# Optimization experiments

Measured on AMD Instinct MI355X. Metric: run time of the kernel, lower is better.

Reference implementation:

```python
import jax, jax.numpy as jnp
import numpy as np

N, E = 10000, 320000
C_IN, C_OUT = 256, 128
EPS = 1e-5


def _p(key, shape, scale=0.02):
    return (jax.random.normal(key, shape, dtype=jnp.float32) * scale)


def setup_inputs() -> dict:
    key = jax.random.key(0)
    ks = jax.random.split(key, 16)
    inp = {
        "x": jax.random.normal(ks[0], (N, C_IN), dtype=jnp.float32),
        "edge_index": jax.random.randint(ks[1], (2, E), 0, N, dtype=jnp.int64),
        # GCNConv weights (stored [in, out] so forward is x @ W)
        "W1": _p(ks[2], (C_IN, C_OUT)), "b1": jnp.zeros((C_OUT,), jnp.float32),
        "W2": _p(ks[3], (C_OUT, C_OUT)), "b2": jnp.zeros((C_OUT,), jnp.float32),
        # LayerNorms
        "ln1_g": jnp.ones((C_OUT,), jnp.float32), "ln1_b": jnp.zeros((C_OUT,), jnp.float32),
        "ln2_g": jnp.ones((C_OUT,), jnp.float32), "ln2_b": jnp.zeros((C_OUT,), jnp.float32),
        # Attention QKV
        "Wq": _p(ks[4], (C_OUT, C_OUT)), "bq": jnp.zeros((C_OUT,), jnp.float32),
        "Wk": _p(ks[5], (C_OUT, C_OUT)), "bk": jnp.zeros((C_OUT,), jnp.float32),
        "Wv": _p(ks[6], (C_OUT, C_OUT)), "bv": jnp.zeros((C_OUT,), jnp.float32),
        # shortcut Linear (in_channels != out_channels)
        "Ws": _p(ks[7], (C_IN, C_OUT)), "bs": jnp.zeros((C_OUT,), jnp.float32),
    }
    return inp


def _gcn_conv(x, W, b, src, dst, n_nodes):
    # PyG GCNConv: h = x W; add self loops; sym-normalized scatter aggregation.
    h = x @ W  # [N, out]
    loop = jnp.arange(n_nodes, dtype=src.dtype)
    s = jnp.concatenate([src, loop])
    d = jnp.concatenate([dst, loop])
    deg = jax.ops.segment_sum(jnp.ones_like(d, dtype=h.dtype), d, num_segments=n_nodes)
    dis = jnp.where(deg > 0, jax.lax.rsqrt(deg), 0.0)  # deg^-1/2
    norm = dis[s] * dis[d]  # [E+N]
    agg = jax.ops.segment_sum(h[s] * norm[:, None], d, num_segments=n_nodes)
    return agg + b


def _layer_norm(x, g, b):
    mu = jnp.mean(x, axis=-1, keepdims=True)
    var = jnp.var(x, axis=-1, keepdims=True)
    return (x - mu) * jax.lax.rsqrt(var + EPS) * g + b


def reference(x, edge_index, W1, b1, W2, b2, ln1_g, ln1_b, ln2_g, ln2_b,
              Wq, bq, Wk, bk, Wv, bv, Ws, bs):
    src, dst = edge_index[0], edge_index[1]
    n = x.shape[0]
    identity = x @ Ws + bs
    out = _gcn_conv(x, W1, b1, src, dst, n)
    out = jax.nn.silu(_layer_norm(out, ln1_g, ln1_b))  # dropout = identity (eval)
    out = _gcn_conv(out, W2, b2, src, dst, n)
    out = _layer_norm(out, ln2_g, ln2_b)
    # dense self-attention over all nodes
    q = out @ Wq + bq
    k = out @ Wk + bk
    v = out @ Wv + bv
    scale = np.sqrt(out.shape[-1]).astype(np.float32)
    attn = jax.nn.softmax(q @ k.T / scale, axis=-1)  # [N, N]
    out = attn @ v + out
    return jax.nn.silu(out + identity)
```

## Files before the change

kernel.cpp:

```cpp
#include <hip/hip_runtime.h>
#include <hip/hip_bf16.h>

typedef unsigned short u16;
typedef unsigned int u32;
typedef __bf16 bf16x8 __attribute__((ext_vector_type(8)));
typedef float f32x4 __attribute__((ext_vector_type(4)));

#define MFMA16(a, b, c) __builtin_amdgcn_mfma_f32_16x16x32_bf16(a, b, c, 0, 0, 0)

static __device__ __forceinline__ u16 f2b(float f) {
  u32 u = __float_as_uint(f);
  return (u16)((u + 0x7FFFu + ((u >> 16) & 1u)) >> 16);
}
static __device__ __forceinline__ float blo(u32 u) { return __uint_as_float(u << 16); }
static __device__ __forceinline__ float bhi(u32 u) { return __uint_as_float(u & 0xffff0000u); }

static __device__ __forceinline__ void async_copy16(void* lds, const void* gp) {
  __builtin_amdgcn_global_load_lds(
      (const __attribute__((address_space(1))) unsigned int*)gp,
      (__attribute__((address_space(3))) unsigned int*)lds, 16, 0, 0);
}

__global__ void degi_kernel(const int* __restrict__ dst, int* __restrict__ degi, int E) {
  int e = blockIdx.x * 256 + threadIdx.x;
  if (e < E) atomicAdd(&degi[dst[e]], 1);
}

__global__ void dis_start_kernel(const int* __restrict__ degi, float* __restrict__ d,
                                 int* __restrict__ startb, int* __restrict__ counter, int N) {
  int i = blockIdx.x * 256 + threadIdx.x;
  if (i < N) {
    int dg = degi[i];
    d[i] = rsqrtf((float)dg + 1.0f);
    startb[i] = atomicAdd(counter, dg);
  }
}

__global__ void fill_kernel(const int* __restrict__ src, const int* __restrict__ dst,
                            const int* __restrict__ startb, int* __restrict__ cursor,
                            int* __restrict__ adj, int E) {
  int e = blockIdx.x * 256 + threadIdx.x;
  if (e < E) {
    int d = dst[e];
    int p = atomicAdd(&cursor[d], 1);
    adj[startb[d] + p] = src[e];
  }
}

__global__ void cast_all_kernel(const float* __restrict__ x, u16* __restrict__ xb, int n4,
                                const float* __restrict__ W1, const float* __restrict__ Ws,
                                const float* __restrict__ W2, const float* __restrict__ Wq,
                                const float* __restrict__ Wk, const float* __restrict__ Wv,
                                u16* __restrict__ out) {
  int t = blockIdx.x * 256 + threadIdx.x;
  if (t < n4) {
    float4 v = *(const float4*)&x[t * 4];
    ushort4 o;
    o.x = f2b(v.x); o.y = f2b(v.y); o.z = f2b(v.z); o.w = f2b(v.w);
    *(ushort4*)&xb[t * 4] = o;
    return;
  }
  int u = t - n4;
  if (u >= 131072) return;
  const float* src; int K, base, loc;
  if (u < 65536) {
    if (u < 32768) { src = W1; base = 0; } else { src = Ws; base = 32768; }
    loc = u - base; K = 256;
  } else {
    int seg = (u - 65536) >> 14;
    src = (seg == 0) ? W2 : (seg == 1) ? Wq : (seg == 2) ? Wk : Wv;
    base = 65536 + seg * 16384; loc = u & 16383; K = 128;
  }
  int k = loc >> 7, c = loc & 127;
  out[base + c * K + k] = f2b(src[loc]);
}

__global__ __launch_bounds__(64) void bgemm_dual(
    const u16* __restrict__ A, const u16* __restrict__ Wa, const u16* __restrict__ Wb,
    const float* __restrict__ bsb, u16* __restrict__ outa, float* __restrict__ outb, int M)
{
  int lane = threadIdx.x;
  int col = lane & 15, quad = lane >> 4;
  int row0 = blockIdx.x * 16;
  int cb = blockIdx.y * 64;
  int ar = row0 + col; if (ar > M - 1) ar = M - 1;
  const u16* ap = A + (size_t)ar * 256 + quad * 8;
  f32x4 Oa[4], Ob[4];
#pragma unroll
  for (int i = 0; i < 4; i++) {
    Oa[i][0] = 0.f; Oa[i][1] = 0.f; Oa[i][2] = 0.f; Oa[i][3] = 0.f;
    Ob[i] = Oa[i];
  }
#pragma unroll
  for (int k0 = 0; k0 < 256; k0 += 32) {
    bf16x8 aA = *(const bf16x8*)(ap + k0);
#pragma unroll
    for (int nb = 0; nb < 4; nb++) {
      size_t wofs = (size_t)(cb + nb * 16 + col) * 256 + k0 + quad * 8;
      Oa[nb] = MFMA16(aA, *(const bf16x8*)(Wa + wofs), Oa[nb]);
      Ob[nb] = MFMA16(aA, *(const bf16x8*)(Wb + wofs), Ob[nb]);
    }
  }
#pragma unroll
  for (int nb = 0; nb < 4; nb++) {
    int ch = cb + nb * 16 + col;
    float bv = bsb[ch];
#pragma unroll
    for (int r = 0; r < 4; r++) {
      int row = row0 + quad * 4 + r;
      if (row >= M) continue;
      outa[(size_t)row * 128 + ch] = f2b(Oa[nb][r]);
      outb[(size_t)row * 128 + ch] = Ob[nb][r] + bv;
    }
  }
}

__global__ __launch_bounds__(64) void bgemm_single(
    const u16* __restrict__ A, const u16* __restrict__ Wt, u16* __restrict__ outa, int M)
{
  int lane = threadIdx.x;
  int col = lane & 15, quad = lane >> 4;
  int row0 = blockIdx.x * 16;
  int cb = blockIdx.y * 64;
  int ar = row0 + col; if (ar > M - 1) ar = M - 1;
  const u16* ap = A + (size_t)ar * 128 + quad * 8;
  f32x4 O[4];
#pragma unroll
  for (int i = 0; i < 4; i++) { O[i][0] = 0.f; O[i][1] = 0.f; O[i][2] = 0.f; O[i][3] = 0.f; }
#pragma unroll
  for (int k0 = 0; k0 < 128; k0 += 32) {
    bf16x8 aA = *(const bf16x8*)(ap + k0);
#pragma unroll
    for (int nb = 0; nb < 4; nb++) {
      O[nb] = MFMA16(aA, *(const bf16x8*)(Wt + (size_t)(cb + nb * 16 + col) * 128 + k0 + quad * 8), O[nb]);
    }
  }
#pragma unroll
  for (int nb = 0; nb < 4; nb++) {
    int ch = cb + nb * 16 + col;
#pragma unroll
    for (int r = 0; r < 4; r++) {
      int row = row0 + quad * 4 + r;
      if (row >= M) continue;
      outa[(size_t)row * 128 + ch] = f2b(O[nb][r]);
    }
  }
}

__global__ __launch_bounds__(64) void bgemm_qkv(
    const u16* __restrict__ A, const u16* __restrict__ Wqt, const u16* __restrict__ Wkt,
    const u16* __restrict__ Wvt, const float* __restrict__ bq, const float* __restrict__ bk,
    const float* __restrict__ bv, u16* __restrict__ q_out, u16* __restrict__ k_out,
    u16* __restrict__ v_out, int M, int NP, float qscale)
{
  int lane = threadIdx.x;
  int col = lane & 15, quad = lane >> 4;
  int row0 = blockIdx.x * 16;
  int cb = blockIdx.y * 64;
  int ar = row0 + col; if (ar > M - 1) ar = M - 1;
  const u16* ap = A + (size_t)ar * 128 + quad * 8;
  f32x4 Oq[4], Ok[4], Ov[4];
#pragma unroll
  for (int i = 0; i < 4; i++) {
    Oq[i][0] = 0.f; Oq[i][1] = 0.f; Oq[i][2] = 0.f; Oq[i][3] = 0.f;
    Ok[i] = Oq[i]; Ov[i] = Oq[i];
  }
#pragma unroll
  for (int k0 = 0; k0 < 128; k0 += 32) {
    bf16x8 aA = *(const bf16x8*)(ap + k0);
#pragma unroll
    for (int nb = 0; nb < 4; nb++) {
      size_t wofs = (size_t)(cb + nb * 16 + col) * 128 + k0 + quad * 8;
      Oq[nb] = MFMA16(aA, *(const bf16x8*)(Wqt + wofs), Oq[nb]);
      Ok[nb] = MFMA16(aA, *(const bf16x8*)(Wkt + wofs), Ok[nb]);
      Ov[nb] = MFMA16(aA, *(const bf16x8*)(Wvt + wofs), Ov[nb]);
    }
  }
#pragma unroll
  for (int nb = 0; nb < 4; nb++) {
    int ch = cb + nb * 16 + col;
    float bqv = bq[ch], bkv = bk[ch], bvv = bv[ch];
#pragma unroll
    for (int r = 0; r < 4; r++) {
      int row = row0 + quad * 4 + r;
      if (row >= M) continue;
      q_out[(size_t)row * 128 + ch] = f2b((Oq[nb][r] + bqv) * qscale);
      k_out[(size_t)row * 128 + ch] = f2b(Ok[nb][r] + bkv);
      v_out[(size_t)ch * NP + row] = f2b(Ov[nb][r] + bvv);
    }
  }
}

__global__ __launch_bounds__(256) void gather_ln(
    const u16* __restrict__ h, const float* __restrict__ dis,
    const int* __restrict__ adj, const int* __restrict__ startb, const int* __restrict__ degi,
    const float* __restrict__ bias, const float* __restrict__ g, const float* __restrict__ beta,
    float* __restrict__ out, u16* __restrict__ outb, int N, int do_silu)
{
  int row = blockIdx.x * 4 + (threadIdx.x >> 6);
  int lane = threadIdx.x & 63;
  if (row >= N) return;
  int st = startb[row], dg = degi[row];
  int c2 = lane * 2;
  float v0 = 0.f, v1 = 0.f;
  for (int base = 0; base < dg; base += 64) {
    int nb = min(64, dg - base);
    int myadj = 0; float mydis = 0.f;
    if (lane < nb) { myadj = adj[st + base + lane]; mydis = dis[myadj]; }
    int jj = 0;
    for (; jj + 4 <= nb; jj += 4) {
      int s0 = __shfl(myadj, jj), s1 = __shfl(myadj, jj + 1);
      int s2 = __shfl(myadj, jj + 2), s3 = __shfl(myadj, jj + 3);
      float w0 = __shfl(mydis, jj), w1 = __shfl(mydis, jj + 1);
      float w2 = __shfl(mydis, jj + 2), w3 = __shfl(mydis, jj + 3);
      u32 a0 = *(const u32*)&h[(size_t)s0 * 128 + c2];
      u32 a1 = *(const u32*)&h[(size_t)s1 * 128 + c2];
      u32 a2 = *(const u32*)&h[(size_t)s2 * 128 + c2];
      u32 a3 = *(const u32*)&h[(size_t)s3 * 128 + c2];
      v0 += w0 * blo(a0); v1 += w0 * bhi(a0);
      v0 += w1 * blo(a1); v1 += w1 * bhi(a1);
      v0 += w2 * blo(a2); v1 += w2 * bhi(a2);
      v0 += w3 * blo(a3); v1 += w3 * bhi(a3);
    }
    for (; jj < nb; jj++) {
      int s = __shfl(myadj, jj);
      float wv = __shfl(mydis, jj);
      u32 a = *(const u32*)&h[(size_t)s * 128 + c2];
      v0 += wv * blo(a); v1 += wv * bhi(a);
    }
  }
  float dd = dis[row];
  u32 aself = *(const u32*)&h[(size_t)row * 128 + c2];
  v0 = (v0 + dd * blo(aself)) * dd + bias[c2];
  v1 = (v1 + dd * bhi(aself)) * dd + bias[c2 + 1];
  float s = v0 + v1;
#pragma unroll
  for (int d = 32; d > 0; d >>= 1) s += __shfl_xor(s, d, 64);
  float mu = s * (1.0f / 128.0f);
  float d0 = v0 - mu, d1 = v1 - mu;
  float q = d0 * d0 + d1 * d1;
#pragma unroll
  for (int d = 32; d > 0; d >>= 1) q += __shfl_xor(q, d, 64);
  float rstd = rsqrtf(q * (1.0f / 128.0f) + 1e-5f);
  float o0 = d0 * rstd * g[c2]     + beta[c2];
  float o1 = d1 * rstd * g[c2 + 1] + beta[c2 + 1];
  if (do_silu) {
    o0 = o0 / (1.f + __expf(-o0));
    o1 = o1 / (1.f + __expf(-o1));
  }
  size_t base = (size_t)row * 128;
  *(float2*)&out[base + c2] = make_float2(o0, o1);
  u32 pk = (u32)f2b(o0) | ((u32)f2b(o1) << 16);
  *(u32*)&outb[base + c2] = pk;
}

__global__ __launch_bounds__(256, 3) void flash_part(
    const u16* __restrict__ qb, const u16* __restrict__ kb, const u16* __restrict__ vt,
    u16* __restrict__ Opart, float* __restrict__ lpart,
    int N, int NP, int CHUNK)
{
  __shared__ __align__(16) u16 Kl[2][32 * 128];
  __shared__ __align__(16) u16 Vl[2][128 * 32];
  __shared__ __align__(16) u16 Pl[4][32][40];
  int tid = threadIdx.x;
  int w = tid >> 6, lane = tid & 63;
  int col = lane & 15, quad = lane >> 4;
  int h8 = col & 7;
  int ks = blockIdx.y;
  int kstart = ks * CHUNK;
  int qbase = blockIdx.x * 128 + w * 32;

  bf16x8 aQ[2][4];
#pragma unroll
  for (int rg = 0; rg < 2; rg++) {
    int qr = qbase + rg * 16 + col; if (qr > N - 1) qr = N - 1;
    const u16* qp = qb + (size_t)qr * 128 + quad * 8;
    aQ[rg][0] = *(const bf16x8*)(qp);
    aQ[rg][1] = *(const bf16x8*)(qp + 32);
    aQ[rg][2] = *(const bf16x8*)(qp + 64);
    aQ[rg][3] = *(const bf16x8*)(qp + 96);
  }

  f32x4 O[2][8];
#pragma unroll
  for (int rg = 0; rg < 2; rg++)
#pragma unroll
    for (int i = 0; i < 8; i++) { O[rg][i][0] = 0.f; O[rg][i][1] = 0.f; O[rg][i][2] = 0.f; O[rg][i][3] = 0.f; }
  float lr[2][4] = {{0.f, 0.f, 0.f, 0.f}, {0.f, 0.f, 0.f, 0.f}};

  int l16 = lane >> 4, c16 = lane & 15;
  int vch = lane >> 2, vc4 = lane & 3;

  auto stage = [&](int buf, int k0) {
#pragma unroll
    for (int i = 0; i < 2; i++) {
      int rl = w * 8 + i * 4 + l16;
      int cg = c16 ^ (rl & 7);
      async_copy16(&Kl[buf][(w * 8 + i * 4) * 128], kb + (size_t)(k0 + rl) * 128 + cg * 8);
    }
#pragma unroll
    for (int i = 0; i < 2; i++) {
      int ch = w * 32 + i * 16 + vch;
      int cg = vc4 ^ ((ch >> 1) & 3);
      async_copy16(&Vl[buf][(w * 32 + i * 16) * 32], vt + (size_t)ch * NP + k0 + cg * 8);
    }
  };

  int KT = (min(CHUNK, NP - kstart)) >> 5;
  stage(0, kstart);

  for (int kt = 0; kt < KT; kt++) {
    int buf = kt & 1;
    int k0 = kstart + (kt << 5);
    asm volatile("s_waitcnt vmcnt(0)\n\ts_barrier" ::: "memory");
    if (kt + 1 < KT) stage(buf ^ 1, k0 + 32);

    const u16* Kb = &Kl[buf][0];
    const u16* Vb = &Vl[buf][0];
    bool edge = (k0 + 32 > N);
#pragma unroll
    for (int g = 0; g < 2; g++) {
      const u16* kr = Kb + (g * 16 + col) * 128;
      bf16x8 kf0 = *(const bf16x8*)(kr + (((0 + quad) ^ h8) << 3));
      bf16x8 kf1 = *(const bf16x8*)(kr + (((4 + quad) ^ h8) << 3));
      bf16x8 kf2 = *(const bf16x8*)(kr + (((8 + quad) ^ h8) << 3));
      bf16x8 kf3 = *(const bf16x8*)(kr + (((12 + quad) ^ h8) << 3));
      f32x4 s0; s0[0] = 0.f; s0[1] = 0.f; s0[2] = 0.f; s0[3] = 0.f;
      f32x4 s1 = s0;
      s0 = MFMA16(aQ[0][0], kf0, s0); s1 = MFMA16(aQ[1][0], kf0, s1);
      s0 = MFMA16(aQ[0][1], kf1, s0); s1 = MFMA16(aQ[1][1], kf1, s1);
      s0 = MFMA16(aQ[0][2], kf2, s0); s1 = MFMA16(aQ[1][2], kf2, s1);
      s0 = MFMA16(aQ[0][3], kf3, s0); s1 = MFMA16(aQ[1][3], kf3, s1);
      if (edge && (k0 + g * 16 + col >= N)) {
        s0[0] = -1e30f; s0[1] = -1e30f; s0[2] = -1e30f; s0[3] = -1e30f;
        s1 = s0;
      }
#pragma unroll
      for (int r = 0; r < 4; r++) {
        float p0 = __expf(s0[r]);
        float p1 = __expf(s1[r]);
        lr[0][r] += p0;
        lr[1][r] += p1;
        Pl[w][quad * 4 + r][g * 16 + col]      = (u16)(__float_as_uint(p0) >> 16);
        Pl[w][16 + quad * 4 + r][g * 16 + col] = (u16)(__float_as_uint(p1) >> 16);
      }
    }
    asm volatile("s_waitcnt lgkmcnt(0)" ::: "memory");
    bf16x8 aP0 = *(const bf16x8*)&Pl[w][col][quad * 8];
    bf16x8 aP1 = *(const bf16x8*)&Pl[w][16 + col][quad * 8];
#pragma unroll
    for (int nb = 0; nb < 8; nb++) {
      int ch = nb * 16 + col;
      const u16* vr = Vb + ch * 32;
      bf16x8 vf = *(const bf16x8*)(vr + ((quad ^ ((ch >> 1) & 3)) << 3));
      O[0][nb] = MFMA16(aP0, vf, O[0][nb]);
      O[1][nb] = MFMA16(aP1, vf, O[1][nb]);
    }
  }

#pragma unroll
  for (int d = 1; d < 16; d <<= 1) {
#pragma unroll
    for (int rg = 0; rg < 2; rg++)
#pragma unroll
      for (int r = 0; r < 4; r++) lr[rg][r] += __shfl_xor(lr[rg][r], d, 64);
  }

#pragma unroll
  for (int rg = 0; rg < 2; rg++) {
#pragma unroll
    for (int nb = 0; nb < 8; nb++) {
      int ch = nb * 16 + col;
#pragma unroll
      for (int r = 0; r < 4; r++) {
        int row = qbase + rg * 16 + quad * 4 + r;
        if (row < N)
          Opart[((size_t)ks * NP + row) * 128 + ch] = f2b(O[rg][nb][r]);
      }
    }
  }
  if (col == 0) {
#pragma unroll
    for (int rg = 0; rg < 2; rg++)
#pragma unroll
      for (int r = 0; r < 4; r++) {
        int row = qbase + rg * 16 + quad * 4 + r;
        if (row < N) lpart[(size_t)ks * NP + row] = lr[rg][r];
      }
  }
}

__global__ __launch_bounds__(256) void attn_combine(
    const u16* __restrict__ Opart, const float* __restrict__ lpart,
    const float* __restrict__ out2, const float* __restrict__ ident, float* __restrict__ out,
    int N, int NP, int S)
{
  int row = blockIdx.x * 2 + (threadIdx.x >> 7);
  int ch = threadIdx.x & 127;
  if (row >= N) return;
  float num = 0.f, den = 0.f;
  for (int u = 0; u < S; u++) {
    u32 b = Opart[((size_t)u * NP + row) * 128 + ch];
    num += __uint_as_float(b << 16);
    den += lpart[(size_t)u * NP + row];
  }
  size_t idx = (size_t)row * 128 + ch;
  float val = num / den + out2[idx] + ident[idx];
  out[idx] = val / (1.f + __expf(-val));
}

extern "C" void kernel_launch(void* const* d_in, const int* in_sizes, int n_in,
                              void* d_out, int out_size, void* d_ws, size_t ws_size,
                              hipStream_t stream) {
  const float* x   = (const float*)d_in[0];
  const int*   ei  = (const int*)d_in[1];
  const float* W1  = (const float*)d_in[2];
  const float* b1  = (const float*)d_in[3];
  const float* W2  = (const float*)d_in[4];
  const float* b2  = (const float*)d_in[5];
  const float* g1  = (const float*)d_in[6];
  const float* be1 = (const float*)d_in[7];
  const float* g2  = (const float*)d_in[8];
  const float* be2 = (const float*)d_in[9];
  const float* Wq  = (const float*)d_in[10];
  const float* bq  = (const float*)d_in[11];
  const float* Wk  = (const float*)d_in[12];
  const float* bk  = (const float*)d_in[13];
  const float* Wv  = (const float*)d_in[14];
  const float* bv  = (const float*)d_in[15];
  const float* Wsw = (const float*)d_in[16];
  const float* bs  = (const float*)d_in[17];

  const int CIN = 256, C = 128;
  int N = in_sizes[0] / CIN;
  int E = in_sizes[1] / 2;
  int NP = (N + 63) & ~63;
  const int* src = ei;
  const int* dstp = ei + E;

  const int S = 8;
  int tiles = NP / 64;
  int CHUNK = ((tiles + S - 1) / S) * 64;

  char* w = (char*)d_ws;
  size_t off = 0;
  auto alloc = [&](size_t bytes) -> void* {
    void* p = w + off;
    off = (off + bytes + 255) & ~(size_t)255;
    return p;
  };
  int*   degi   = (int*)alloc((size_t)N * 4);
  int*   cursor = (int*)alloc((size_t)N * 4);
  int*   counter= (int*)alloc(256);
  size_t zlen   = off;
  float* disb   = (float*)alloc((size_t)N * 4);
  int*   startb = (int*)alloc((size_t)N * 4);
  int*   adj    = (int*)alloc((size_t)E * 4);
  u16*   h      = (u16*)alloc((size_t)N * C * 2);
  float* ident  = (float*)alloc((size_t)N * C * 4);
  float* cur    = (float*)alloc((size_t)N * C * 4);
  u16*   xb     = (u16*)alloc((size_t)N * CIN * 2);
  u16*   curb   = (u16*)alloc((size_t)N * C * 2);
  u16*   wt     = (u16*)alloc((size_t)131072 * 2);
  u16*   qbb    = (u16*)alloc((size_t)N * C * 2);
  u16*   kbb    = (u16*)alloc((size_t)NP * C * 2);
  u16*   vt     = (u16*)alloc((size_t)C * NP * 2);
  u16*   Opart  = (u16*)alloc((size_t)S * NP * C * 2);
  float* lpart  = (float*)alloc((size_t)S * NP * 4);

  u16* wt1 = wt;
  u16* wts = wt + 32768;
  u16* wt2 = wt + 65536;
  u16* wtq = wt + 81920;
  u16* wtk = wt + 98304;
  u16* wtv = wt + 114688;

  hipMemsetAsync(degi, 0, zlen, stream);

  int gE = (E + 255) / 256, gN = (N + 255) / 256;
  degi_kernel<<<gE, 256, 0, stream>>>(dstp, degi, E);
  dis_start_kernel<<<gN, 256, 0, stream>>>(degi, disb, startb, counter, N);
  fill_kernel<<<gE, 256, 0, stream>>>(src, dstp, startb, cursor, adj, E);

  int n4 = N * CIN / 4;
  int ctot = n4 + 131072;
  cast_all_kernel<<<(ctot + 255) / 256, 256, 0, stream>>>(x, xb, n4, W1, Wsw, W2, Wq, Wk, Wv, wt);

  dim3 gbg((N + 15) / 16, 2);
  bgemm_dual<<<gbg, 64, 0, stream>>>(xb, wt1, wts, bs, h, ident, N);
  gather_ln<<<(N + 3) / 4, 256, 0, stream>>>(h, disb, adj, startb, degi, b1, g1, be1, cur, curb, N, 1);
  bgemm_single<<<gbg, 64, 0, stream>>>(curb, wt2, h, N);
  gather_ln<<<(N + 3) / 4, 256, 0, stream>>>(h, disb, adj, startb, degi, b2, g2, be2, cur, curb, N, 0);

  const float qscale = 0.08838834764831845f;
  bgemm_qkv<<<gbg, 64, 0, stream>>>(curb, wtq, wtk, wtv, bq, bk, bv, qbb, kbb, vt, N, NP, qscale);

  dim3 fg((N + 127) / 128, S);
  flash_part<<<fg, 256, 0, stream>>>(qbb, kbb, vt, Opart, lpart, N, NP, CHUNK);
  attn_combine<<<(N + 1) / 2, 256, 0, stream>>>(Opart, lpart, cur, ident,
                                                (float*)d_out, N, NP, S);
}
```

Measured before the change: 293.9 us.

## Use wave-scan CSR offsets, deeper gather unroll, exp2 softmax, vectorized combine

```diff
diff --git a/kernel.cpp b/kernel.cpp
--- a/kernel.cpp
+++ b/kernel.cpp
@@ -29,11 +29,20 @@
 __global__ void dis_start_kernel(const int* __restrict__ degi, float* __restrict__ d,
                                  int* __restrict__ startb, int* __restrict__ counter, int N) {
   int i = blockIdx.x * 256 + threadIdx.x;
-  if (i < N) {
-    int dg = degi[i];
-    d[i] = rsqrtf((float)dg + 1.0f);
-    startb[i] = atomicAdd(counter, dg);
-  }
+  int lane = threadIdx.x & 63;
+  int dg = (i < N) ? degi[i] : 0;
+  if (i < N) d[i] = rsqrtf((float)dg + 1.0f);
+  int x = dg;
+#pragma unroll
+  for (int ofs = 1; ofs < 64; ofs <<= 1) {
+    int y = __shfl_up(x, ofs, 64);
+    if (lane >= ofs) x += y;
+  }
+  int waveTotal = __shfl(x, 63, 64);
+  int base = 0;
+  if (lane == 63) base = atomicAdd(counter, waveTotal);
+  base = __shfl(base, 63, 64);
+  if (i < N) startb[i] = base + x - dg;
 }
 
 __global__ void fill_kernel(const int* __restrict__ src, const int* __restrict__ dst,
@@ -208,19 +217,31 @@
     int myadj = 0; float mydis = 0.f;
     if (lane < nb) { myadj = adj[st + base + lane]; mydis = dis[myadj]; }
     int jj = 0;
-    for (; jj + 4 <= nb; jj += 4) {
-      int s0 = __shfl(myadj, jj), s1 = __shfl(myadj, jj + 1);
+    for (; jj + 8 <= nb; jj += 8) {
+      int s0 = __shfl(myadj, jj),     s1 = __shfl(myadj, jj + 1);
       int s2 = __shfl(myadj, jj + 2), s3 = __shfl(myadj, jj + 3);
-      float w0 = __shfl(mydis, jj), w1 = __shfl(mydis, jj + 1);
+      int s4 = __shfl(myadj, jj + 4), s5 = __shfl(myadj, jj + 5);
+      int s6 = __shfl(myadj, jj + 6), s7 = __shfl(myadj, jj + 7);
+      float w0 = __shfl(mydis, jj),     w1 = __shfl(mydis, jj + 1);
       float w2 = __shfl(mydis, jj + 2), w3 = __shfl(mydis, jj + 3);
+      float w4 = __shfl(mydis, jj + 4), w5 = __shfl(mydis, jj + 5);
+      float w6 = __shfl(mydis, jj + 6), w7 = __shfl(mydis, jj + 7);
       u32 a0 = *(const u32*)&h[(size_t)s0 * 128 + c2];
       u32 a1 = *(const u32*)&h[(size_t)s1 * 128 + c2];
       u32 a2 = *(const u32*)&h[(size_t)s2 * 128 + c2];
       u32 a3 = *(const u32*)&h[(size_t)s3 * 128 + c2];
+      u32 a4 = *(const u32*)&h[(size_t)s4 * 128 + c2];
+      u32 a5 = *(const u32*)&h[(size_t)s5 * 128 + c2];
+      u32 a6 = *(const u32*)&h[(size_t)s6 * 128 + c2];
+      u32 a7 = *(const u32*)&h[(size_t)s7 * 128 + c2];
       v0 += w0 * blo(a0); v1 += w0 * bhi(a0);
       v0 += w1 * blo(a1); v1 += w1 * bhi(a1);
       v0 += w2 * blo(a2); v1 += w2 * bhi(a2);
       v0 += w3 * blo(a3); v1 += w3 * bhi(a3);
+      v0 += w4 * blo(a4); v1 += w4 * bhi(a4);
+      v0 += w5 * blo(a5); v1 += w5 * bhi(a5);
+      v0 += w6 * blo(a6); v1 += w6 * bhi(a6);
+      v0 += w7 * blo(a7); v1 += w7 * bhi(a7);
     }
     for (; jj < nb; jj++) {
       int s = __shfl(myadj, jj);
@@ -337,8 +358,8 @@
       }
 #pragma unroll
       for (int r = 0; r < 4; r++) {
-        float p0 = __expf(s0[r]);
-        float p1 = __expf(s1[r]);
+        float p0 = exp2f(s0[r]);
+        float p1 = exp2f(s1[r]);
         lr[0][r] += p0;
         lr[1][r] += p1;
         Pl[w][quad * 4 + r][g * 16 + col]      = (u16)(__float_as_uint(p0) >> 16);
@@ -395,18 +416,24 @@
     const float* __restrict__ out2, const float* __restrict__ ident, float* __restrict__ out,
     int N, int NP, int S)
 {
-  int row = blockIdx.x * 2 + (threadIdx.x >> 7);
-  int ch = threadIdx.x & 127;
+  int row = blockIdx.x * 4 + (threadIdx.x >> 6);
+  int c2 = (threadIdx.x & 63) * 2;
   if (row >= N) return;
-  float num = 0.f, den = 0.f;
+  float num0 = 0.f, num1 = 0.f, den = 0.f;
   for (int u = 0; u < S; u++) {
-    u32 b = Opart[((size_t)u * NP + row) * 128 + ch];
-    num += __uint_as_float(b << 16);
+    u32 b = *(const u32*)&Opart[((size_t)u * NP + row) * 128 + c2];
+    num0 += blo(b); num1 += bhi(b);
     den += lpart[(size_t)u * NP + row];
   }
-  size_t idx = (size_t)row * 128 + ch;
-  float val = num / den + out2[idx] + ident[idx];
-  out[idx] = val / (1.f + __expf(-val));
+  size_t idx = (size_t)row * 128 + c2;
+  float rinv = 1.0f / den;
+  float2 o2 = *(const float2*)&out2[idx];
+  float2 id = *(const float2*)&ident[idx];
+  float v0 = num0 * rinv + o2.x + id.x;
+  float v1 = num1 * rinv + o2.y + id.y;
+  v0 = v0 / (1.f + __expf(-v0));
+  v1 = v1 / (1.f + __expf(-v1));
+  *(float2*)&out[idx] = make_float2(v0, v1);
 }
 
 extern "C" void kernel_launch(void* const* d_in, const int* in_sizes, int n_in,
@@ -492,11 +519,11 @@
   bgemm_single<<<gbg, 64, 0, stream>>>(curb, wt2, h, N);
   gather_ln<<<(N + 3) / 4, 256, 0, stream>>>(h, disb, adj, startb, degi, b2, g2, be2, cur, curb, N, 0);
 
-  const float qscale = 0.08838834764831845f;
+  const float qscale = 0.12753224f;
   bgemm_qkv<<<gbg, 64, 0, stream>>>(curb, wtq, wtk, wtv, bq, bk, bv, qbb, kbb, vt, N, NP, qscale);
 
   dim3 fg((N + 127) / 128, S);
   flash_part<<<fg, 256, 0, stream>>>(qbb, kbb, vt, Opart, lpart, N, NP, CHUNK);
-  attn_combine<<<(N + 1) / 2, 256, 0, stream>>>(Opart, lpart, cur, ident,
+  attn_combine<<<(N + 3) / 4, 256, 0, stream>>>(Opart, lpart, cur, ident,
                                                 (float*)d_out, N, NP, S);
 }
```

After: 299.8 us. 2.0% more time.
